# Optimization experiments

Measured on AMD Instinct MI355X. Metric: run time of the kernel, lower is better.

The kernel has to match this reference:

```python
import jax, jax.numpy as jnp
import numpy as np

N_HEADS = 12

def setup_inputs() -> dict:
    key = jax.random.key(0)
    ks = jax.random.split(key, 6)
    B, S, C = 8, 1024, 768
    x = jax.random.normal(ks[0], (B, S, C), dtype=jnp.float32)
    attention_mask = jnp.ones((B, S), dtype=jnp.int32)
    scale = 1.0 / np.sqrt(C)
    w_qkv = jax.random.normal(ks[1], (3 * C, C), dtype=jnp.float32) * scale
    b_qkv = jnp.zeros((3 * C,), dtype=jnp.float32)
    w_out = jax.random.normal(ks[2], (C, C), dtype=jnp.float32) * scale
    b_out = jnp.zeros((C,), dtype=jnp.float32)
    return {"x": x, "w_qkv": w_qkv, "b_qkv": b_qkv, "w_out": w_out,
            "b_out": b_out, "attention_mask": attention_mask}


def reference(x, w_qkv, b_qkv, w_out, b_out, attention_mask):
    B, S, C = x.shape
    H = N_HEADS
    D = C // H
    qkv = x @ w_qkv.T + b_qkv                      # [B,S,3C]
    q, k, v = jnp.split(qkv, 3, axis=2)
    # [B,S,C] -> [B,H,S,D]
    q = q.reshape(B, S, H, D).transpose(0, 2, 1, 3)
    k = k.reshape(B, S, H, D).transpose(0, 2, 1, 3)
    v = v.reshape(B, S, H, D).transpose(0, 2, 1, 3)
    att = jnp.einsum('bhsd,bhtd->bhst', q, k) / np.sqrt(D).astype(jnp.float32)
    causal = jnp.tril(jnp.ones((S, S), dtype=bool))[None, None]      # [1,1,S,S]
    key_mask = attention_mask.astype(bool)[:, None, None, :]        # [B,1,1,S]
    mask = causal & key_mask                                        # [B,1,S,S]
    neg = jnp.finfo(att.dtype).min
    att = jnp.where(mask, att, neg)
    att = jax.nn.softmax(att, axis=-1)
    att = jnp.where(mask, att, 0.0)                                 # second masked_fill
    y = jnp.einsum('bhst,bhtd->bhsd', att, v)                       # [B,H,S,D]
    y = y.transpose(0, 2, 1, 3).reshape(B, S, C)
    return y @ w_out.T + b_out
```

## Files before the change

kernel.cpp:

```cpp
#include <hip/hip_runtime.h>
#include <hip/hip_bf16.h>
#include <math.h>

#define BATCH 8
#define SEQ   1024
#define CDIM  768
#define NH    12
#define HD    64
#define M_TOT (BATCH * SEQ)
#define N_QKV (3 * CDIM)
#define KDIM  768

typedef __attribute__((ext_vector_type(4))) _Float16 half4;
typedef __attribute__((ext_vector_type(8))) _Float16 half8;
typedef __attribute__((ext_vector_type(4))) float floatx4;

__device__ __forceinline__ void gld_lds16(const _Float16* g, _Float16* l) {
    __builtin_amdgcn_global_load_lds(
        (const __attribute__((address_space(1))) void*)g,
        (__attribute__((address_space(3))) void*)l, 16, 0, 0);
}

__global__ __launch_bounds__(256) void cvt_f32_f16(
    const float* __restrict__ src, _Float16* __restrict__ dst)
{
    const size_t i = ((size_t)blockIdx.x * 256 + threadIdx.x) * 4;
    float4 v = *reinterpret_cast<const float4*>(src + i);
    half4 h;
    h[0] = (_Float16)v.x; h[1] = (_Float16)v.y;
    h[2] = (_Float16)v.z; h[3] = (_Float16)v.w;
    *reinterpret_cast<half4*>(dst + i) = h;
}

__global__ __launch_bounds__(256) void gemm_qkv(
    const _Float16* __restrict__ A, const _Float16* __restrict__ B,
    const float* __restrict__ bias, _Float16* __restrict__ C)
{
    __shared__ _Float16 Atile[128 * 64];
    __shared__ _Float16 Btile[128 * 64];
    const int tid  = threadIdx.x;
    const int wave = tid >> 6, lane = tid & 63, quad = lane >> 4, l16 = lane & 15;
    const int wm = wave >> 1, wn = wave & 1;
    const int m0 = blockIdx.y * 128, n0 = blockIdx.x * 128;

    const int strow = tid >> 3;
    const int scg   = (tid & 7) ^ (strow & 7);
    const _Float16* gA = A + (size_t)(m0 + strow) * KDIM + scg * 8;
    const _Float16* gB = B + (size_t)(n0 + strow) * KDIM + scg * 8;
    _Float16* lA = Atile + tid * 8;
    _Float16* lB = Btile + tid * 8;

    floatx4 acc[4][4];
#pragma unroll
    for (int i = 0; i < 4; ++i)
#pragma unroll
        for (int j = 0; j < 4; ++j) acc[i][j] = (floatx4){0.f, 0.f, 0.f, 0.f};

    for (int k0 = 0; k0 < KDIM; k0 += 64) {
        __syncthreads();
#pragma unroll
        for (int i = 0; i < 4; ++i) {
            gld_lds16(gA + (size_t)(i * 32) * KDIM + k0, lA + i * 2048);
            gld_lds16(gB + (size_t)(i * 32) * KDIM + k0, lB + i * 2048);
        }
        __syncthreads();
#pragma unroll
        for (int kk = 0; kk < 2; ++kk) {
            const int cg = (quad + kk * 4) ^ (l16 & 7);
            half8 aF[4], bF[4];
#pragma unroll
            for (int mt = 0; mt < 4; ++mt)
                aF[mt] = *reinterpret_cast<const half8*>(
                    &Atile[(wm * 64 + mt * 16 + l16) * 64 + cg * 8]);
#pragma unroll
            for (int nt = 0; nt < 4; ++nt)
                bF[nt] = *reinterpret_cast<const half8*>(
                    &Btile[(wn * 64 + nt * 16 + l16) * 64 + cg * 8]);
#pragma unroll
            for (int mt = 0; mt < 4; ++mt)
#pragma unroll
                for (int nt = 0; nt < 4; ++nt)
                    acc[mt][nt] = __builtin_amdgcn_mfma_f32_16x16x32_f16(
                        aF[mt], bF[nt], acc[mt][nt], 0, 0, 0);
        }
    }

#pragma unroll
    for (int nt = 0; nt < 4; ++nt) {
        const int col = n0 + wn * 64 + nt * 16 + l16;
        const float bv = bias[col];
#pragma unroll
        for (int mt = 0; mt < 4; ++mt) {
            const int rowb = m0 + wm * 64 + mt * 16 + quad * 4;
#pragma unroll
            for (int r = 0; r < 4; ++r)
                C[(size_t)(rowb + r) * N_QKV + col] = (_Float16)(acc[mt][nt][r] + bv);
        }
    }
}

__global__ __launch_bounds__(256) void gemm_out(
    const _Float16* __restrict__ A, const _Float16* __restrict__ B,
    const float* __restrict__ bias, float* __restrict__ C)
{
    __shared__ _Float16 Atile[64 * 64];
    __shared__ _Float16 Btile[128 * 64];
    const int tid  = threadIdx.x;
    const int wave = tid >> 6, lane = tid & 63, quad = lane >> 4, l16 = lane & 15;
    const int m0 = blockIdx.y * 64, n0 = blockIdx.x * 128;

    const int strow = tid >> 3;
    const int scg   = (tid & 7) ^ (strow & 7);
    const _Float16* gA = A + (size_t)(m0 + strow) * KDIM + scg * 8;
    const _Float16* gB = B + (size_t)(n0 + strow) * KDIM + scg * 8;
    _Float16* lA = Atile + tid * 8;
    _Float16* lB = Btile + tid * 8;

    floatx4 acc[8];
#pragma unroll
    for (int i = 0; i < 8; ++i) acc[i] = (floatx4){0.f, 0.f, 0.f, 0.f};

    for (int k0 = 0; k0 < KDIM; k0 += 64) {
        __syncthreads();
        gld_lds16(gA + k0, lA);
        gld_lds16(gA + (size_t)32 * KDIM + k0, lA + 2048);
#pragma unroll
        for (int i = 0; i < 4; ++i)
            gld_lds16(gB + (size_t)(i * 32) * KDIM + k0, lB + i * 2048);
        __syncthreads();
#pragma unroll
        for (int kk = 0; kk < 2; ++kk) {
            const int cg = (quad + kk * 4) ^ (l16 & 7);
            half8 aF = *reinterpret_cast<const half8*>(
                &Atile[(wave * 16 + l16) * 64 + cg * 8]);
            half8 bF[8];
#pragma unroll
            for (int nt = 0; nt < 8; ++nt)
                bF[nt] = *reinterpret_cast<const half8*>(
                    &Btile[(nt * 16 + l16) * 64 + cg * 8]);
#pragma unroll
            for (int nt = 0; nt < 8; ++nt)
                acc[nt] = __builtin_amdgcn_mfma_f32_16x16x32_f16(
                    aF, bF[nt], acc[nt], 0, 0, 0);
        }
    }

#pragma unroll
    for (int nt = 0; nt < 8; ++nt) {
        const int col = n0 + nt * 16 + l16;
        const float bv = bias[col];
        const int rowb = m0 + wave * 16 + quad * 4;
#pragma unroll
        for (int r = 0; r < 4; ++r)
            C[(size_t)(rowb + r) * CDIM + col] = acc[nt][r] + bv;
    }
}

__global__ __launch_bounds__(256) void transpose_v(
    const _Float16* __restrict__ QKV, _Float16* __restrict__ VT)
{
    __shared__ _Float16 t[64][73];
    const int s0 = blockIdx.x * 64, h = blockIdx.y, b = blockIdx.z;
    const int tid = threadIdx.x;
#pragma unroll
    for (int it = 0; it < 2; ++it) {
        const int s = it * 32 + (tid >> 3);
        const int d8 = (tid & 7) * 8;
        half8 v = *reinterpret_cast<const half8*>(
            QKV + (size_t)(b * SEQ + s0 + s) * N_QKV + 2 * CDIM + h * HD + d8);
#pragma unroll
        for (int i = 0; i < 8; ++i) t[s][d8 + i] = v[i];
    }
    __syncthreads();
#pragma unroll
    for (int it = 0; it < 2; ++it) {
        const int d = it * 32 + (tid >> 3);
        const int s8 = (tid & 7) * 8;
        half8 o;
#pragma unroll
        for (int i = 0; i < 8; ++i) o[i] = t[s8 + i][d];
        *reinterpret_cast<half8*>(
            VT + ((size_t)(b * NH + h) * HD + d) * SEQ + s0 + s8) = o;
    }
}

__global__ __launch_bounds__(256) void flash_attn(
    const _Float16* __restrict__ QKV, const _Float16* __restrict__ VT,
    const int* __restrict__ amask, _Float16* __restrict__ Y)
{
    __shared__ __align__(16) char smraw[36864];
    _Float16 (*Klds)[64][72] = (_Float16 (*)[64][72])smraw;
    _Float16 (*Vlds)[64][68] = (_Float16 (*)[64][68])(smraw + 18432);
    float (*kmb)[64] = (float (*)[64])(smraw + 35840);
    _Float16 (*osm)[72] = (_Float16 (*)[72])smraw;

    const int qt = blockIdx.x;
    const int h  = blockIdx.y;
    const int b  = blockIdx.z;
    const int tid = threadIdx.x;
    const int w = tid >> 6, lane = tid & 63, quad = lane >> 4, l16 = lane & 15;
    const int qbA = qt * 64;
    const int qbB = (15 - qt) * 64;

    int qi[2];
    qi[0] = qbA + w * 16 + l16;
    qi[1] = qbB + w * 16 + l16;

    half8 qf[2][2];
#pragma unroll
    for (int qg = 0; qg < 2; ++qg)
#pragma unroll
        for (int kc = 0; kc < 2; ++kc) {
            half8 q = *reinterpret_cast<const half8*>(
                QKV + (size_t)(b * SEQ + qi[qg]) * N_QKV + h * HD + kc * 32 + quad * 8);
#pragma unroll
            for (int i = 0; i < 8; ++i) q[i] = q[i] * (_Float16)0.125f;
            qf[qg][kc] = q;
        }

    float rsum[2] = {0.f, 0.f};
    floatx4 accO[2][4];
#pragma unroll
    for (int qg = 0; qg < 2; ++qg)
#pragma unroll
        for (int dt = 0; dt < 4; ++dt) accO[qg][dt] = (floatx4){0.f, 0.f, 0.f, 0.f};

    const int srow = tid >> 2;
    const int sc16 = (tid & 3) * 16;
    const _Float16* gK = QKV + ((size_t)(b * SEQ + srow)) * N_QKV + CDIM + h * HD + sc16;
    const _Float16* gV = VT + ((size_t)(b * NH + h) * HD + srow) * SEQ + sc16;

    const int nt = 16 - qt;

    half8 kr0 = *reinterpret_cast<const half8*>(gK);
    half8 kr1 = *reinterpret_cast<const half8*>(gK + 8);
    half8 vr0 = *reinterpret_cast<const half8*>(gV);
    half8 vr1 = *reinterpret_cast<const half8*>(gV + 8);
    float kmr = 0.f;
    if (tid < 64) kmr = amask[b * SEQ + tid] ? 0.f : -1e30f;

    for (int t = 0; t < nt; ++t) {
        const int buf = t & 1;
        const int t0 = t * 64;
        const bool actA  = (t <= qt);
        const bool fullA = (t < qt);
        const bool fullB = (t + qt < 15);

        *reinterpret_cast<half8*>(&Klds[buf][srow][sc16])     = kr0;
        *reinterpret_cast<half8*>(&Klds[buf][srow][sc16 + 8]) = kr1;
        *reinterpret_cast<half8*>(&Vlds[buf][srow][sc16])     = vr0;
        *reinterpret_cast<half8*>(&Vlds[buf][srow][sc16 + 8]) = vr1;
        if (tid < 64) kmb[buf][tid] = kmr;
        __syncthreads();

        if (t + 1 < nt) {
            const int t1 = (t + 1) * 64;
            kr0 = *reinterpret_cast<const half8*>(gK + (size_t)t1 * N_QKV);
            kr1 = *reinterpret_cast<const half8*>(gK + (size_t)t1 * N_QKV + 8);
            vr0 = *reinterpret_cast<const half8*>(gV + t1);
            vr1 = *reinterpret_cast<const half8*>(gV + t1 + 8);
            if (tid < 64) kmr = amask[b * SEQ + t1 + tid] ? 0.f : -1e30f;
        }

        float4 bias4[4];
#pragma unroll
        for (int kt = 0; kt < 4; ++kt)
            bias4[kt] = *reinterpret_cast<const float4*>(&kmb[buf][kt * 16 + quad * 4]);

        half4 pfA[4], pfB[4];
#pragma unroll
        for (int kt = 0; kt < 4; ++kt) {
            floatx4 aS0 = (floatx4){0.f, 0.f, 0.f, 0.f};
            floatx4 aS1 = (floatx4){0.f, 0.f, 0.f, 0.f};
#pragma unroll
            for (int kc = 0; kc < 2; ++kc) {
                half8 kf = *reinterpret_cast<const half8*>(
                    &Klds[buf][kt * 16 + l16][kc * 32 + quad * 8]);
                if (actA) aS0 = __builtin_amdgcn_mfma_f32_16x16x32_f16(kf, qf[0][kc], aS0, 0, 0, 0);
                aS1 = __builtin_amdgcn_mfma_f32_16x16x32_f16(kf, qf[1][kc], aS1, 0, 0, 0);
            }
#pragma unroll
            for (int r = 0; r < 4; ++r) {
                const int key = t0 + kt * 16 + quad * 4 + r;
                const float bias = bias4[kt][r];
                if (actA) {
                    float sA = aS0[r] + bias;
                    if (!fullA && key > qi[0]) sA = -1e30f;
                    const float pA = __expf(sA);
                    rsum[0] += pA;
                    pfA[kt][r] = (_Float16)pA;
                }
                float sB = aS1[r] + bias;
                if (!fullB && key > qi[1]) sB = -1e30f;
                const float pB = __expf(sB);
                rsum[1] += pB;
                pfB[kt][r] = (_Float16)pB;
            }
        }

#pragma unroll
        for (int dt = 0; dt < 4; ++dt) {
#pragma unroll
            for (int kt = 0; kt < 4; ++kt) {
                half4 vf = *reinterpret_cast<const half4*>(
                    &Vlds[buf][dt * 16 + l16][kt * 16 + quad * 4]);
                if (actA) accO[0][dt] = __builtin_amdgcn_mfma_f32_16x16x16f16(
                    vf, pfA[kt], accO[0][dt], 0, 0, 0);
                accO[1][dt] = __builtin_amdgcn_mfma_f32_16x16x16f16(
                    vf, pfB[kt], accO[1][dt], 0, 0, 0);
            }
        }
    }

    float inv[2];
#pragma unroll
    for (int qg = 0; qg < 2; ++qg) {
        float l = rsum[qg];
        l += __shfl_xor(l, 16, 64);
        l += __shfl_xor(l, 32, 64);
        inv[qg] = (l > 0.f) ? 1.f / l : 0.f;
    }

    __syncthreads();
#pragma unroll
    for (int qg = 0; qg < 2; ++qg)
#pragma unroll
        for (int dt = 0; dt < 4; ++dt)
#pragma unroll
            for (int r = 0; r < 4; ++r)
                osm[qg * 64 + w * 16 + l16][dt * 16 + quad * 4 + r] =
                    (_Float16)(accO[qg][dt][r] * inv[qg]);
    __syncthreads();

    const int q  = tid >> 1;
    const int dc = (tid & 1) * 32;
    const int grow = (q < 64) ? (qbA + q) : (qbB + q - 64);
    _Float16* dst = Y + ((size_t)(b * SEQ + grow)) * CDIM + h * HD + dc;
#pragma unroll
    for (int i = 0; i < 4; ++i)
        *reinterpret_cast<half8*>(dst + 8 * i) =
            *reinterpret_cast<const half8*>(&osm[q][dc + 8 * i]);
}

extern "C" void kernel_launch(void* const* d_in, const int* in_sizes, int n_in,
                              void* d_out, int out_size, void* d_ws, size_t ws_size,
                              hipStream_t stream)
{
    const float* x      = (const float*)d_in[0];
    const float* w_qkv  = (const float*)d_in[1];
    const float* b_qkv  = (const float*)d_in[2];
    const float* w_out  = (const float*)d_in[3];
    const float* b_out  = (const float*)d_in[4];
    const int*   amask  = (const int*)d_in[5];
    float* out = (float*)d_out;

    _Float16* ws = (_Float16*)d_ws;
    _Float16* x16    = ws;
    _Float16* wqkv16 = x16 + (size_t)M_TOT * CDIM;
    _Float16* wout16 = wqkv16 + (size_t)N_QKV * CDIM;
    _Float16* qkv16  = wout16 + (size_t)CDIM * CDIM;
    _Float16* y16    = qkv16 + (size_t)M_TOT * N_QKV;
    _Float16* VT     = y16 + (size_t)M_TOT * CDIM;

    cvt_f32_f16<<<(M_TOT * CDIM) / 1024, 256, 0, stream>>>(x, x16);
    cvt_f32_f16<<<(N_QKV * CDIM) / 1024, 256, 0, stream>>>(w_qkv, wqkv16);
    cvt_f32_f16<<<(CDIM * CDIM) / 1024, 256, 0, stream>>>(w_out, wout16);

    gemm_qkv<<<dim3(N_QKV / 128, M_TOT / 128), 256, 0, stream>>>(
        x16, wqkv16, b_qkv, qkv16);
    transpose_v<<<dim3(SEQ / 64, NH, BATCH), 256, 0, stream>>>(qkv16, VT);
    flash_attn<<<dim3(8, NH, BATCH), 256, 0, stream>>>(
        qkv16, VT, amask, y16);
    gemm_out<<<dim3(CDIM / 128, M_TOT / 64), 256, 0, stream>>>(
        y16, wout16, b_out, out);
}
```

Before: 214.0 us.

## Fuse conversions, write V transposed from QKV GEMM, async LDS loads in attention

Merges the three fp32->fp16 conversion launches into one kernel. The QKV GEMM epilogue now writes V directly in transposed layout, so the separate transpose kernel goes away. Flash attention stages K/V tiles with global_load_lds into XOR-swizzled LDS instead of register round-trips, reads the key mask straight into registers, and folds log2(e) into the Q scale so it can use exp2. Packed fp16 conversion replaces the scalar casts. The risks are uncoalesced 8-byte strided VT stores in the GEMM epilogue and the fixed block-index thresholds in the merged conversion kernel.

Result: faster. 200.3 us (-6.4%).

```diff
diff --git a/kernel.cpp b/kernel.cpp
--- a/kernel.cpp
+++ b/kernel.cpp
@@ -21,10 +21,26 @@
         (__attribute__((address_space(3))) void*)l, 16, 0, 0);
 }
 
-__global__ __launch_bounds__(256) void cvt_f32_f16(
-    const float* __restrict__ src, _Float16* __restrict__ dst)
-{
-    const size_t i = ((size_t)blockIdx.x * 256 + threadIdx.x) * 4;
+__device__ __forceinline__ float exp2_fast(float x) {
+#if __has_builtin(__builtin_amdgcn_exp2f)
+    return __builtin_amdgcn_exp2f(x);
+#else
+    float r; asm("v_exp_f32 %0, %1" : "=v"(r) : "v"(x)); return r;
+#endif
+}
+
+__global__ __launch_bounds__(256) void cvt_all(
+    const float* __restrict__ x, const float* __restrict__ wq,
+    const float* __restrict__ wo,
+    _Float16* __restrict__ x16, _Float16* __restrict__ wq16,
+    _Float16* __restrict__ wo16)
+{
+    const int bid = blockIdx.x;
+    const float* src; _Float16* dst; size_t base;
+    if (bid < 6144)      { src = x;  dst = x16;  base = (size_t)bid * 1024; }
+    else if (bid < 7872) { src = wq; dst = wq16; base = (size_t)(bid - 6144) * 1024; }
+    else                 { src = wo; dst = wo16; base = (size_t)(bid - 7872) * 1024; }
+    const size_t i = base + threadIdx.x * 4;
     float4 v = *reinterpret_cast<const float4*>(src + i);
     half4 h;
     h[0] = (_Float16)v.x; h[1] = (_Float16)v.y;
@@ -34,7 +50,8 @@
 
 __global__ __launch_bounds__(256) void gemm_qkv(
     const _Float16* __restrict__ A, const _Float16* __restrict__ B,
-    const float* __restrict__ bias, _Float16* __restrict__ C)
+    const float* __restrict__ bias, _Float16* __restrict__ C,
+    _Float16* __restrict__ VT)
 {
     __shared__ _Float16 Atile[128 * 64];
     __shared__ _Float16 Btile[128 * 64];
@@ -85,16 +102,37 @@
         }
     }
 
-#pragma unroll
-    for (int nt = 0; nt < 4; ++nt) {
-        const int col = n0 + wn * 64 + nt * 16 + l16;
-        const float bv = bias[col];
-#pragma unroll
-        for (int mt = 0; mt < 4; ++mt) {
-            const int rowb = m0 + wm * 64 + mt * 16 + quad * 4;
-#pragma unroll
-            for (int r = 0; r < 4; ++r)
-                C[(size_t)(rowb + r) * N_QKV + col] = (_Float16)(acc[mt][nt][r] + bv);
+    if (n0 < 2 * CDIM) {
+#pragma unroll
+        for (int nt = 0; nt < 4; ++nt) {
+            const int col = n0 + wn * 64 + nt * 16 + l16;
+            const float bv = bias[col];
+#pragma unroll
+            for (int mt = 0; mt < 4; ++mt) {
+                const int rowb = m0 + wm * 64 + mt * 16 + quad * 4;
+#pragma unroll
+                for (int r = 0; r < 4; ++r)
+                    C[(size_t)(rowb + r) * N_QKV + col] = (_Float16)(acc[mt][nt][r] + bv);
+            }
+        }
+    } else {
+        const int bb = m0 >> 10;
+#pragma unroll
+        for (int nt = 0; nt < 4; ++nt) {
+            const int colf = n0 + wn * 64 + nt * 16 + l16;
+            const float bv = bias[colf];
+            const int hd = colf - 2 * CDIM;
+            const int hh = hd >> 6, d = hd & 63;
+#pragma unroll
+            for (int mt = 0; mt < 4; ++mt) {
+                const int rowb = m0 + wm * 64 + mt * 16 + quad * 4;
+                const int s = rowb & 1023;
+                half4 hv;
+#pragma unroll
+                for (int r = 0; r < 4; ++r) hv[r] = (_Float16)(acc[mt][nt][r] + bv);
+                *reinterpret_cast<half4*>(
+                    &VT[((size_t)(bb * NH + hh) * HD + d) * SEQ + s]) = hv;
+            }
         }
     }
 }
@@ -156,56 +194,22 @@
     }
 }
 
-__global__ __launch_bounds__(256) void transpose_v(
-    const _Float16* __restrict__ QKV, _Float16* __restrict__ VT)
-{
-    __shared__ _Float16 t[64][73];
-    const int s0 = blockIdx.x * 64, h = blockIdx.y, b = blockIdx.z;
-    const int tid = threadIdx.x;
-#pragma unroll
-    for (int it = 0; it < 2; ++it) {
-        const int s = it * 32 + (tid >> 3);
-        const int d8 = (tid & 7) * 8;
-        half8 v = *reinterpret_cast<const half8*>(
-            QKV + (size_t)(b * SEQ + s0 + s) * N_QKV + 2 * CDIM + h * HD + d8);
-#pragma unroll
-        for (int i = 0; i < 8; ++i) t[s][d8 + i] = v[i];
-    }
-    __syncthreads();
-#pragma unroll
-    for (int it = 0; it < 2; ++it) {
-        const int d = it * 32 + (tid >> 3);
-        const int s8 = (tid & 7) * 8;
-        half8 o;
-#pragma unroll
-        for (int i = 0; i < 8; ++i) o[i] = t[s8 + i][d];
-        *reinterpret_cast<half8*>(
-            VT + ((size_t)(b * NH + h) * HD + d) * SEQ + s0 + s8) = o;
-    }
-}
-
 __global__ __launch_bounds__(256) void flash_attn(
     const _Float16* __restrict__ QKV, const _Float16* __restrict__ VT,
     const int* __restrict__ amask, _Float16* __restrict__ Y)
 {
-    __shared__ __align__(16) char smraw[36864];
-    _Float16 (*Klds)[64][72] = (_Float16 (*)[64][72])smraw;
-    _Float16 (*Vlds)[64][68] = (_Float16 (*)[64][68])(smraw + 18432);
-    float (*kmb)[64] = (float (*)[64])(smraw + 35840);
-    _Float16 (*osm)[72] = (_Float16 (*)[72])smraw;
-
-    const int qt = blockIdx.x;
-    const int h  = blockIdx.y;
-    const int b  = blockIdx.z;
+    __shared__ __align__(16) char smraw[32768];
+    _Float16 (*Klds)[4096] = (_Float16 (*)[4096])smraw;
+    _Float16 (*Vlds)[4096] = (_Float16 (*)[4096])(smraw + 16384);
+    _Float16 (*osm)[72]    = (_Float16 (*)[72])smraw;
+
+    const int qt = blockIdx.x, h = blockIdx.y, b = blockIdx.z;
     const int tid = threadIdx.x;
     const int w = tid >> 6, lane = tid & 63, quad = lane >> 4, l16 = lane & 15;
-    const int qbA = qt * 64;
-    const int qbB = (15 - qt) * 64;
-
-    int qi[2];
-    qi[0] = qbA + w * 16 + l16;
-    qi[1] = qbB + w * 16 + l16;
-
+    const int qbA = qt * 64, qbB = (15 - qt) * 64;
+    int qi[2] = { qbA + w * 16 + l16, qbB + w * 16 + l16 };
+
+    const _Float16 qscale = (_Float16)0.18033688f;
     half8 qf[2][2];
 #pragma unroll
     for (int qg = 0; qg < 2; ++qg)
@@ -214,7 +218,7 @@
             half8 q = *reinterpret_cast<const half8*>(
                 QKV + (size_t)(b * SEQ + qi[qg]) * N_QKV + h * HD + kc * 32 + quad * 8);
 #pragma unroll
-            for (int i = 0; i < 8; ++i) q[i] = q[i] * (_Float16)0.125f;
+            for (int i = 0; i < 8; ++i) q[i] = q[i] * qscale;
             qf[qg][kc] = q;
         }
 
@@ -225,90 +229,112 @@
 #pragma unroll
         for (int dt = 0; dt < 4; ++dt) accO[qg][dt] = (floatx4){0.f, 0.f, 0.f, 0.f};
 
-    const int srow = tid >> 2;
-    const int sc16 = (tid & 3) * 16;
-    const _Float16* gK = QKV + ((size_t)(b * SEQ + srow)) * N_QKV + CDIM + h * HD + sc16;
-    const _Float16* gV = VT + ((size_t)(b * NH + h) * HD + srow) * SEQ + sc16;
+    const int srow0 = w * 16 + (lane >> 3);
+    const int scg   = ((lane & 7) ^ (srow0 & 7)) * 8;
+    const _Float16* gK = QKV + ((size_t)b * SEQ + srow0) * N_QKV + CDIM + h * HD + scg;
+    const _Float16* gV = VT + ((size_t)(b * NH + h) * HD + srow0) * SEQ + scg;
 
     const int nt = 16 - qt;
 
-    half8 kr0 = *reinterpret_cast<const half8*>(gK);
-    half8 kr1 = *reinterpret_cast<const half8*>(gK + 8);
-    half8 vr0 = *reinterpret_cast<const half8*>(gV);
-    half8 vr1 = *reinterpret_cast<const half8*>(gV + 8);
-    float kmr = 0.f;
-    if (tid < 64) kmr = amask[b * SEQ + tid] ? 0.f : -1e30f;
+    gld_lds16(gK,             &Klds[0][w * 1024]);
+    gld_lds16(gK + 8 * N_QKV, &Klds[0][w * 1024 + 512]);
+    gld_lds16(gV,             &Vlds[0][w * 1024]);
+    gld_lds16(gV + 8 * SEQ,   &Vlds[0][w * 1024 + 512]);
+    int4 mcur[4];
+#pragma unroll
+    for (int kt = 0; kt < 4; ++kt)
+        mcur[kt] = *reinterpret_cast<const int4*>(&amask[b * SEQ + kt * 16 + quad * 4]);
 
     for (int t = 0; t < nt; ++t) {
-        const int buf = t & 1;
+        const int buf = t & 1, nbuf = buf ^ 1;
         const int t0 = t * 64;
-        const bool actA  = (t <= qt);
-        const bool fullA = (t < qt);
-        const bool fullB = (t + qt < 15);
-
-        *reinterpret_cast<half8*>(&Klds[buf][srow][sc16])     = kr0;
-        *reinterpret_cast<half8*>(&Klds[buf][srow][sc16 + 8]) = kr1;
-        *reinterpret_cast<half8*>(&Vlds[buf][srow][sc16])     = vr0;
-        *reinterpret_cast<half8*>(&Vlds[buf][srow][sc16 + 8]) = vr1;
-        if (tid < 64) kmb[buf][tid] = kmr;
-        __syncthreads();
-
+        const bool actA = (t <= qt), fullA = (t < qt), fullB = (t + qt < 15);
+
+        __syncthreads();
+
+        int4 mnext[4];
         if (t + 1 < nt) {
-            const int t1 = (t + 1) * 64;
-            kr0 = *reinterpret_cast<const half8*>(gK + (size_t)t1 * N_QKV);
-            kr1 = *reinterpret_cast<const half8*>(gK + (size_t)t1 * N_QKV + 8);
-            vr0 = *reinterpret_cast<const half8*>(gV + t1);
-            vr1 = *reinterpret_cast<const half8*>(gV + t1 + 8);
-            if (tid < 64) kmr = amask[b * SEQ + t1 + tid] ? 0.f : -1e30f;
-        }
-
-        float4 bias4[4];
-#pragma unroll
-        for (int kt = 0; kt < 4; ++kt)
-            bias4[kt] = *reinterpret_cast<const float4*>(&kmb[buf][kt * 16 + quad * 4]);
+            const int t1 = t0 + 64;
+            gld_lds16(gK + (size_t)t1 * N_QKV,       &Klds[nbuf][w * 1024]);
+            gld_lds16(gK + (size_t)(t1 + 8) * N_QKV, &Klds[nbuf][w * 1024 + 512]);
+            gld_lds16(gV + t1,                       &Vlds[nbuf][w * 1024]);
+            gld_lds16(gV + t1 + 8 * SEQ,             &Vlds[nbuf][w * 1024 + 512]);
+#pragma unroll
+            for (int kt = 0; kt < 4; ++kt)
+                mnext[kt] = *reinterpret_cast<const int4*>(
+                    &amask[b * SEQ + t1 + kt * 16 + quad * 4]);
+        }
+
+        float bias[4][4];
+#pragma unroll
+        for (int kt = 0; kt < 4; ++kt) {
+            bias[kt][0] = mcur[kt].x ? 0.f : -1e30f;
+            bias[kt][1] = mcur[kt].y ? 0.f : -1e30f;
+            bias[kt][2] = mcur[kt].z ? 0.f : -1e30f;
+            bias[kt][3] = mcur[kt].w ? 0.f : -1e30f;
+        }
 
         half4 pfA[4], pfB[4];
 #pragma unroll
         for (int kt = 0; kt < 4; ++kt) {
             floatx4 aS0 = (floatx4){0.f, 0.f, 0.f, 0.f};
             floatx4 aS1 = (floatx4){0.f, 0.f, 0.f, 0.f};
+            const int krow = kt * 16 + l16;
 #pragma unroll
             for (int kc = 0; kc < 2; ++kc) {
                 half8 kf = *reinterpret_cast<const half8*>(
-                    &Klds[buf][kt * 16 + l16][kc * 32 + quad * 8]);
+                    &Klds[buf][krow * 64 + (((kc * 4 + quad) ^ (krow & 7)) * 8)]);
                 if (actA) aS0 = __builtin_amdgcn_mfma_f32_16x16x32_f16(kf, qf[0][kc], aS0, 0, 0, 0);
                 aS1 = __builtin_amdgcn_mfma_f32_16x16x32_f16(kf, qf[1][kc], aS1, 0, 0, 0);
             }
+            float pA[4], pB[4];
 #pragma unroll
             for (int r = 0; r < 4; ++r) {
                 const int key = t0 + kt * 16 + quad * 4 + r;
-                const float bias = bias4[kt][r];
+                float sB = aS1[r] + bias[kt][r];
+                if (!fullB && key > qi[1]) sB = -1e30f;
+                pB[r] = exp2_fast(sB);
                 if (actA) {
-                    float sA = aS0[r] + bias;
+                    float sA = aS0[r] + bias[kt][r];
                     if (!fullA && key > qi[0]) sA = -1e30f;
-                    const float pA = __expf(sA);
-                    rsum[0] += pA;
-                    pfA[kt][r] = (_Float16)pA;
+                    pA[r] = exp2_fast(sA);
                 }
-                float sB = aS1[r] + bias;
-                if (!fullB && key > qi[1]) sB = -1e30f;
-                const float pB = __expf(sB);
-                rsum[1] += pB;
-                pfB[kt][r] = (_Float16)pB;
+            }
+            rsum[1] += (pB[0] + pB[1]) + (pB[2] + pB[3]);
+            {
+                auto lo = __builtin_amdgcn_cvt_pkrtz(pB[0], pB[1]);
+                auto hi = __builtin_amdgcn_cvt_pkrtz(pB[2], pB[3]);
+                half4 pf; pf[0] = lo[0]; pf[1] = lo[1]; pf[2] = hi[0]; pf[3] = hi[1];
+                pfB[kt] = pf;
+            }
+            if (actA) {
+                rsum[0] += (pA[0] + pA[1]) + (pA[2] + pA[3]);
+                auto lo = __builtin_amdgcn_cvt_pkrtz(pA[0], pA[1]);
+                auto hi = __builtin_amdgcn_cvt_pkrtz(pA[2], pA[3]);
+                half4 pf; pf[0] = lo[0]; pf[1] = lo[1]; pf[2] = hi[0]; pf[3] = hi[1];
+                pfA[kt] = pf;
             }
         }
 
 #pragma unroll
         for (int dt = 0; dt < 4; ++dt) {
+            const int vrow = dt * 16 + l16;
 #pragma unroll
             for (int kt = 0; kt < 4; ++kt) {
                 half4 vf = *reinterpret_cast<const half4*>(
-                    &Vlds[buf][dt * 16 + l16][kt * 16 + quad * 4]);
+                    &Vlds[buf][vrow * 64 +
+                               (((kt * 2 + (quad >> 1)) ^ (vrow & 7)) * 8) +
+                               (quad & 1) * 4]);
                 if (actA) accO[0][dt] = __builtin_amdgcn_mfma_f32_16x16x16f16(
                     vf, pfA[kt], accO[0][dt], 0, 0, 0);
                 accO[1][dt] = __builtin_amdgcn_mfma_f32_16x16x16f16(
                     vf, pfB[kt], accO[1][dt], 0, 0, 0);
             }
+        }
+
+        if (t + 1 < nt) {
+#pragma unroll
+            for (int kt = 0; kt < 4; ++kt) mcur[kt] = mnext[kt];
         }
     }
 
@@ -362,13 +388,10 @@
     _Float16* y16    = qkv16 + (size_t)M_TOT * N_QKV;
     _Float16* VT     = y16 + (size_t)M_TOT * CDIM;
 
-    cvt_f32_f16<<<(M_TOT * CDIM) / 1024, 256, 0, stream>>>(x, x16);
-    cvt_f32_f16<<<(N_QKV * CDIM) / 1024, 256, 0, stream>>>(w_qkv, wqkv16);
-    cvt_f32_f16<<<(CDIM * CDIM) / 1024, 256, 0, stream>>>(w_out, wout16);
+    cvt_all<<<8448, 256, 0, stream>>>(x, w_qkv, w_out, x16, wqkv16, wout16);
 
     gemm_qkv<<<dim3(N_QKV / 128, M_TOT / 128), 256, 0, stream>>>(
-        x16, wqkv16, b_qkv, qkv16);
-    transpose_v<<<dim3(SEQ / 64, NH, BATCH), 256, 0, stream>>>(qkv16, VT);
+        x16, wqkv16, b_qkv, qkv16, VT);
     flash_attn<<<dim3(8, NH, BATCH), 256, 0, stream>>>(
         qkv16, VT, amask, y16);
     gemm_out<<<dim3(CDIM / 128, M_TOT / 64), 256, 0, stream>>>(
```
